# Performance work log

Hardware: AMD Instinct MI355X
Metric: run time of the kernel (lower is better)

The kernel has to match this reference:

```python
import jax, jax.numpy as jnp
import numpy as np


def setup_inputs() -> dict:
    key = jax.random.key(0)
    k1, k2 = jax.random.split(key)
    B, N, C = 4, 4096, 128
    points = jax.random.normal(k1, (B, N, 3), dtype=jnp.float32)
    features = jax.random.normal(k2, (B, C, N), dtype=jnp.float32)
    return {"points": points, "features": features, "npoint": 1024}


def _square_dist(a, b):
    # a: [B, N, D], b: [B, M, D] -> [B, N, M], norm=False (no division by D)
    aa = jnp.sum(a * a, axis=-1)  # [B, N]
    bb = jnp.sum(b * b, axis=-1)  # [B, M]
    ab = jnp.einsum('bnd,bmd->bnm', a, b)  # [B, N, M]
    return aa[:, :, None] + bb[:, None, :] - 2.0 * ab


def _fps_with_dist(dist, npoint):
    # dist: [B, N, N] pairwise squared distances; sequential furthest-point selection
    B, N, _ = dist.shape

    def step(carry, _):
        mind, last = carry  # mind: [B, N] min dist to selected set; last: [B] last picked idx
        d = jnp.take_along_axis(dist, last[:, None, None], axis=1)[:, 0, :]  # [B, N]
        mind = jnp.minimum(mind, d)
        nxt = jnp.argmax(mind, axis=1).astype(jnp.int32)
        return (mind, nxt), last

    init = (jnp.full((B, N), 1e10, dtype=dist.dtype), jnp.zeros((B,), jnp.int32))
    _, idxs = jax.lax.scan(step, init, None, length=npoint)  # [npoint, B]
    return idxs.T  # [B, npoint]


def reference(points, features, npoint):
    # features_for_fps = cat([points, features^T], dim=2): [B, N, 3 + C]
    f = jnp.concatenate([points, jnp.swapaxes(features, 1, 2)], axis=2)
    dist = _square_dist(f, f)  # [B, N, N]
    return _fps_with_dist(dist, npoint)
```

## Files before the change

kernel.cpp:

```cpp
#include <hip/hip_runtime.h>

#define BB 4
#define NN 4096
#define CC 128
#define DD 131
#define NPOINT 1024

__device__ __forceinline__ float fmul_(float a, float b) { return __fmul_rn(a, b); }
__device__ __forceinline__ float fadd_(float a, float b) { return __fadd_rn(a, b); }

__device__ float aa_xla_vf8ic4(const float* __restrict__ row) {
    float p[4][8];
#pragma unroll
    for (int j = 0; j < 4; ++j)
#pragma unroll
        for (int l = 0; l < 8; ++l)
            p[j][l] = fmul_(row[8 * j + l], row[8 * j + l]);
#pragma unroll
    for (int it = 1; it < 4; ++it)
#pragma unroll
        for (int j = 0; j < 4; ++j)
#pragma unroll
            for (int l = 0; l < 8; ++l) {
                float x = row[32 * it + 8 * j + l];
                p[j][l] = fadd_(p[j][l], fmul_(x, x));
            }
    float v[8];
#pragma unroll
    for (int l = 0; l < 8; ++l)
        v[l] = fadd_(fadd_(fadd_(p[0][l], p[1][l]), p[2][l]), p[3][l]);
    float h4_0 = fadd_(v[0], v[4]), h4_1 = fadd_(v[1], v[5]);
    float h4_2 = fadd_(v[2], v[6]), h4_3 = fadd_(v[3], v[7]);
    float h2_0 = fadd_(h4_0, h4_2), h2_1 = fadd_(h4_1, h4_3);
    float h1 = fadd_(h2_0, h2_1);
    h1 = fadd_(h1, fmul_(row[128], row[128]));
    h1 = fadd_(h1, fmul_(row[129], row[129]));
    h1 = fadd_(h1, fmul_(row[130], row[130]));
    return h1;
}

__global__ __launch_bounds__(256) void dist_kernel(const float* __restrict__ points,
                                                   const float* __restrict__ features,
                                                   float* __restrict__ dist) {
    __shared__ float At[64][132];
    __shared__ float Bt[32][132];
    __shared__ float s_aai[64];
    __shared__ float s_aaj[32];

    const int b  = blockIdx.z;
    const int i0 = blockIdx.x * 64;
    const int j0 = blockIdx.y * 32;
    const int tid = threadIdx.x;

    {
        const int rA = tid & 63, gA = tid >> 6;
        for (int k = gA; k < DD; k += 4) {
            float v;
            if (k < 3) v = points[((size_t)b * NN + i0 + rA) * 3 + k];
            else       v = features[((size_t)b * CC + (k - 3)) * NN + i0 + rA];
            At[rA][k] = v;
        }
        const int rB = tid & 31, gB = tid >> 5;
        for (int k = gB; k < DD; k += 8) {
            float v;
            if (k < 3) v = points[((size_t)b * NN + j0 + rB) * 3 + k];
            else       v = features[((size_t)b * CC + (k - 3)) * NN + j0 + rB];
            Bt[rB][k] = v;
        }
    }
    __syncthreads();

    if (tid < 64)        s_aai[tid]      = aa_xla_vf8ic4(At[tid]);
    else if (tid < 96)   s_aaj[tid - 64] = aa_xla_vf8ic4(Bt[tid - 64]);
    __syncthreads();

    const int tx = tid & 15;
    const int ty = tid >> 4;

    float acc[4][2];
#pragma unroll
    for (int p = 0; p < 4; ++p) { acc[p][0] = 0.f; acc[p][1] = 0.f; }

    for (int kb = 0; kb < 128; kb += 4) {
        float4 a0 = *(const float4*)&At[4 * ty + 0][kb];
        float4 a1 = *(const float4*)&At[4 * ty + 1][kb];
        float4 a2 = *(const float4*)&At[4 * ty + 2][kb];
        float4 a3 = *(const float4*)&At[4 * ty + 3][kb];
        float4 b0 = *(const float4*)&Bt[2 * tx + 0][kb];
        float4 b1 = *(const float4*)&Bt[2 * tx + 1][kb];
        const float4 av[4] = {a0, a1, a2, a3};
        const float4 bv[2] = {b0, b1};
#pragma unroll
        for (int p = 0; p < 4; ++p)
#pragma unroll
            for (int q = 0; q < 2; ++q) {
                float s = acc[p][q];
                s = __builtin_fmaf(av[p].x, bv[q].x, s);
                s = __builtin_fmaf(av[p].y, bv[q].y, s);
                s = __builtin_fmaf(av[p].z, bv[q].z, s);
                s = __builtin_fmaf(av[p].w, bv[q].w, s);
                acc[p][q] = s;
            }
    }
#pragma unroll
    for (int p = 0; p < 4; ++p)
#pragma unroll
        for (int q = 0; q < 2; ++q) {
            float s = acc[p][q];
            s = __builtin_fmaf(At[4 * ty + p][128], Bt[2 * tx + q][128], s);
            s = __builtin_fmaf(At[4 * ty + p][129], Bt[2 * tx + q][129], s);
            s = __builtin_fmaf(At[4 * ty + p][130], Bt[2 * tx + q][130], s);
            acc[p][q] = s;
        }

#pragma unroll
    for (int p = 0; p < 4; ++p) {
        const int i = i0 + 4 * ty + p;
        float2 st;
        st.x = __builtin_fmaf(-2.0f, acc[p][0],
                              fadd_(s_aai[4 * ty + p], s_aaj[2 * tx + 0]));
        st.y = __builtin_fmaf(-2.0f, acc[p][1],
                              fadd_(s_aai[4 * ty + p], s_aaj[2 * tx + 1]));
        *(float2*)&dist[((size_t)b * NN + i) * NN + j0 + 2 * tx] = st;
    }
}

__global__ __launch_bounds__(256) void fps_kernel(const float* __restrict__ dist,
                                                  int* __restrict__ out) {
    const int b = blockIdx.x;
    const int tid = threadIdx.x;
    const int lane = tid & 63;
    const int wave = tid >> 6;
    const float* Dm = dist + (size_t)b * NN * NN;

    __shared__ float s_val[2][4];
    __shared__ int   s_idx[2][4];

    float4 mind[4];
#pragma unroll
    for (int c = 0; c < 4; ++c) mind[c] = make_float4(1e10f, 1e10f, 1e10f, 1e10f);
    int last = 0;

    for (int k = 0; k < NPOINT; ++k) {
        if (tid == 0) out[b * NPOINT + k] = last;

        const float* row = Dm + (size_t)last * NN;
        float4 d[4];
#pragma unroll
        for (int c = 0; c < 4; ++c)
            d[c] = *(const float4*)&row[c * 1024 + 4 * tid];

#pragma unroll
        for (int c = 0; c < 4; ++c) {
            mind[c].x = fminf(mind[c].x, d[c].x);
            mind[c].y = fminf(mind[c].y, d[c].y);
            mind[c].z = fminf(mind[c].z, d[c].z);
            mind[c].w = fminf(mind[c].w, d[c].w);
        }

        float bv = mind[0].x; int bi = 4 * tid;
#pragma unroll
        for (int c = 0; c < 4; ++c) {
            const int base = c * 1024 + 4 * tid;
            const float* m = &mind[c].x;
#pragma unroll
            for (int e = 0; e < 4; ++e) {
                if (c == 0 && e == 0) continue;
                if (m[e] > bv) { bv = m[e]; bi = base + e; }
            }
        }

#pragma unroll
        for (int m = 32; m >= 1; m >>= 1) {
            float ov = __shfl_xor(bv, m, 64);
            int   oi = __shfl_xor(bi, m, 64);
            if (ov > bv || (ov == bv && oi < bi)) { bv = ov; bi = oi; }
        }

        const int p = k & 1;
        if (lane == 0) { s_val[p][wave] = bv; s_idx[p][wave] = bi; }
        __syncthreads();

        float v = s_val[p][lane & 3];
        int  ii = s_idx[p][lane & 3];
#pragma unroll
        for (int m = 2; m >= 1; m >>= 1) {
            float ov = __shfl_xor(v, m, 64);
            int   oi = __shfl_xor(ii, m, 64);
            if (ov > v || (ov == v && oi < ii)) { v = ov; ii = oi; }
        }
        last = ii;
    }
}

extern "C" void kernel_launch(void* const* d_in, const int* in_sizes, int n_in,
                              void* d_out, int out_size, void* d_ws, size_t ws_size,
                              hipStream_t stream) {
    const float* points   = (const float*)d_in[0];
    const float* features = (const float*)d_in[1];
    int* out = (int*)d_out;

    float* dist = (float*)d_ws;

    dim3 g(NN / 64, NN / 32, BB);
    dist_kernel<<<g, 256, 0, stream>>>(points, features, dist);

    fps_kernel<<<BB, 256, 0, stream>>>(dist, out);
}
```

Measured before the change: 1.838 ms.

## Retile distance GEMM to 64x64 k-major tiles and single-wave FPS

The distance kernel now uses 64x64 output tiles held k-major in shared memory and splits the 131-wide reduction into two staged halves. Each thread computes a 4x4 block and writes float4 stores. The squared-norm sums are computed in the same order as before, so results should be bit-identical. The FPS kernel drops from four waves to one wave per batch, with each lane holding 64 min-distances; this removes the per-iteration __syncthreads and cross-wave reduction but serialises more load and compare work per lane.

Measured after the change: 2.303 ms. +25.3%, slower.

```diff
diff --git a/kernel.cpp b/kernel.cpp
--- a/kernel.cpp
+++ b/kernel.cpp
@@ -9,159 +9,174 @@
 __device__ __forceinline__ float fmul_(float a, float b) { return __fmul_rn(a, b); }
 __device__ __forceinline__ float fadd_(float a, float b) { return __fadd_rn(a, b); }
 
-__device__ float aa_xla_vf8ic4(const float* __restrict__ row) {
-    float p[4][8];
-#pragma unroll
-    for (int j = 0; j < 4; ++j)
-#pragma unroll
-        for (int l = 0; l < 8; ++l)
-            p[j][l] = fmul_(row[8 * j + l], row[8 * j + l]);
-#pragma unroll
-    for (int it = 1; it < 4; ++it)
-#pragma unroll
-        for (int j = 0; j < 4; ++j)
-#pragma unroll
-            for (int l = 0; l < 8; ++l) {
-                float x = row[32 * it + 8 * j + l];
-                p[j][l] = fadd_(p[j][l], fmul_(x, x));
-            }
-    float v[8];
-#pragma unroll
-    for (int l = 0; l < 8; ++l)
-        v[l] = fadd_(fadd_(fadd_(p[0][l], p[1][l]), p[2][l]), p[3][l]);
-    float h4_0 = fadd_(v[0], v[4]), h4_1 = fadd_(v[1], v[5]);
-    float h4_2 = fadd_(v[2], v[6]), h4_3 = fadd_(v[3], v[7]);
-    float h2_0 = fadd_(h4_0, h4_2), h2_1 = fadd_(h4_1, h4_3);
-    float h1 = fadd_(h2_0, h2_1);
-    h1 = fadd_(h1, fmul_(row[128], row[128]));
-    h1 = fadd_(h1, fmul_(row[129], row[129]));
-    h1 = fadd_(h1, fmul_(row[130], row[130]));
-    return h1;
-}
-
 __global__ __launch_bounds__(256) void dist_kernel(const float* __restrict__ points,
                                                    const float* __restrict__ features,
                                                    float* __restrict__ dist) {
-    __shared__ float At[64][132];
-    __shared__ float Bt[32][132];
+    __shared__ float As[67][64];
+    __shared__ float Bs[67][64];
     __shared__ float s_aai[64];
-    __shared__ float s_aaj[32];
+    __shared__ float s_aaj[64];
 
     const int b  = blockIdx.z;
     const int i0 = blockIdx.x * 64;
-    const int j0 = blockIdx.y * 32;
+    const int j0 = blockIdx.y * 64;
     const int tid = threadIdx.x;
-
-    {
-        const int rA = tid & 63, gA = tid >> 6;
-        for (int k = gA; k < DD; k += 4) {
-            float v;
-            if (k < 3) v = points[((size_t)b * NN + i0 + rA) * 3 + k];
-            else       v = features[((size_t)b * CC + (k - 3)) * NN + i0 + rA];
-            At[rA][k] = v;
-        }
-        const int rB = tid & 31, gB = tid >> 5;
-        for (int k = gB; k < DD; k += 8) {
-            float v;
-            if (k < 3) v = points[((size_t)b * NN + j0 + rB) * 3 + k];
-            else       v = features[((size_t)b * CC + (k - 3)) * NN + j0 + rB];
-            Bt[rB][k] = v;
-        }
-    }
-    __syncthreads();
-
-    if (tid < 64)        s_aai[tid]      = aa_xla_vf8ic4(At[tid]);
-    else if (tid < 96)   s_aaj[tid - 64] = aa_xla_vf8ic4(Bt[tid - 64]);
-    __syncthreads();
-
+    const int r = tid & 63, g = tid >> 6;
     const int tx = tid & 15;
     const int ty = tid >> 4;
 
-    float acc[4][2];
-#pragma unroll
-    for (int p = 0; p < 4; ++p) { acc[p][0] = 0.f; acc[p][1] = 0.f; }
-
-    for (int kb = 0; kb < 128; kb += 4) {
-        float4 a0 = *(const float4*)&At[4 * ty + 0][kb];
-        float4 a1 = *(const float4*)&At[4 * ty + 1][kb];
-        float4 a2 = *(const float4*)&At[4 * ty + 2][kb];
-        float4 a3 = *(const float4*)&At[4 * ty + 3][kb];
-        float4 b0 = *(const float4*)&Bt[2 * tx + 0][kb];
-        float4 b1 = *(const float4*)&Bt[2 * tx + 1][kb];
-        const float4 av[4] = {a0, a1, a2, a3};
-        const float4 bv[2] = {b0, b1};
+    for (int k = g; k < 64; k += 4) {
+        float av, bv;
+        if (k < 3) {
+            av = points[((size_t)b * NN + i0 + r) * 3 + k];
+            bv = points[((size_t)b * NN + j0 + r) * 3 + k];
+        } else {
+            const float* frow = features + ((size_t)b * CC + (k - 3)) * NN;
+            av = frow[i0 + r];
+            bv = frow[j0 + r];
+        }
+        As[k][r] = av;
+        Bs[k][r] = bv;
+    }
+    __syncthreads();
+
+    float ph[4][8];
+    if (tid < 128) {
+        const int rr = tid & 63;
+        const float (*S)[64] = (tid < 64) ? As : Bs;
+#pragma unroll
+        for (int j = 0; j < 4; ++j)
+#pragma unroll
+            for (int l = 0; l < 8; ++l) {
+                float x = S[8 * j + l][rr];
+                ph[j][l] = fmul_(x, x);
+            }
+#pragma unroll
+        for (int j = 0; j < 4; ++j)
+#pragma unroll
+            for (int l = 0; l < 8; ++l) {
+                float x = S[32 + 8 * j + l][rr];
+                ph[j][l] = fadd_(ph[j][l], fmul_(x, x));
+            }
+    }
+
+    float acc[4][4];
+#pragma unroll
+    for (int p = 0; p < 4; ++p)
+#pragma unroll
+        for (int q = 0; q < 4; ++q) acc[p][q] = 0.f;
+
+#pragma unroll 4
+    for (int kk = 0; kk < 64; ++kk) {
+        float4 a4 = *(const float4*)&As[kk][4 * ty];
+        float4 b4 = *(const float4*)&Bs[kk][4 * tx];
+        const float a[4] = {a4.x, a4.y, a4.z, a4.w};
+        const float c[4] = {b4.x, b4.y, b4.z, b4.w};
 #pragma unroll
         for (int p = 0; p < 4; ++p)
 #pragma unroll
-            for (int q = 0; q < 2; ++q) {
-                float s = acc[p][q];
-                s = __builtin_fmaf(av[p].x, bv[q].x, s);
-                s = __builtin_fmaf(av[p].y, bv[q].y, s);
-                s = __builtin_fmaf(av[p].z, bv[q].z, s);
-                s = __builtin_fmaf(av[p].w, bv[q].w, s);
-                acc[p][q] = s;
-            }
-    }
-#pragma unroll
-    for (int p = 0; p < 4; ++p)
-#pragma unroll
-        for (int q = 0; q < 2; ++q) {
-            float s = acc[p][q];
-            s = __builtin_fmaf(At[4 * ty + p][128], Bt[2 * tx + q][128], s);
-            s = __builtin_fmaf(At[4 * ty + p][129], Bt[2 * tx + q][129], s);
-            s = __builtin_fmaf(At[4 * ty + p][130], Bt[2 * tx + q][130], s);
-            acc[p][q] = s;
-        }
+            for (int q = 0; q < 4; ++q)
+                acc[p][q] = __builtin_fmaf(a[p], c[q], acc[p][q]);
+    }
+    __syncthreads();
+
+    for (int k = g; k < 67; k += 4) {
+        const float* frow = features + ((size_t)b * CC + (64 + k - 3)) * NN;
+        As[k][r] = frow[i0 + r];
+        Bs[k][r] = frow[j0 + r];
+    }
+    __syncthreads();
+
+    if (tid < 128) {
+        const int rr = tid & 63;
+        const float (*S)[64] = (tid < 64) ? As : Bs;
+#pragma unroll
+        for (int j = 0; j < 4; ++j)
+#pragma unroll
+            for (int l = 0; l < 8; ++l) {
+                float x = S[8 * j + l][rr];
+                ph[j][l] = fadd_(ph[j][l], fmul_(x, x));
+            }
+#pragma unroll
+        for (int j = 0; j < 4; ++j)
+#pragma unroll
+            for (int l = 0; l < 8; ++l) {
+                float x = S[32 + 8 * j + l][rr];
+                ph[j][l] = fadd_(ph[j][l], fmul_(x, x));
+            }
+        float v[8];
+#pragma unroll
+        for (int l = 0; l < 8; ++l)
+            v[l] = fadd_(fadd_(fadd_(ph[0][l], ph[1][l]), ph[2][l]), ph[3][l]);
+        float h4_0 = fadd_(v[0], v[4]), h4_1 = fadd_(v[1], v[5]);
+        float h4_2 = fadd_(v[2], v[6]), h4_3 = fadd_(v[3], v[7]);
+        float h1 = fadd_(fadd_(h4_0, h4_2), fadd_(h4_1, h4_3));
+        float t0 = S[64][rr], t1 = S[65][rr], t2 = S[66][rr];
+        h1 = fadd_(h1, fmul_(t0, t0));
+        h1 = fadd_(h1, fmul_(t1, t1));
+        h1 = fadd_(h1, fmul_(t2, t2));
+        if (tid < 64) s_aai[rr] = h1; else s_aaj[rr] = h1;
+    }
+
+#pragma unroll 4
+    for (int kk = 0; kk < 67; ++kk) {
+        float4 a4 = *(const float4*)&As[kk][4 * ty];
+        float4 b4 = *(const float4*)&Bs[kk][4 * tx];
+        const float a[4] = {a4.x, a4.y, a4.z, a4.w};
+        const float c[4] = {b4.x, b4.y, b4.z, b4.w};
+#pragma unroll
+        for (int p = 0; p < 4; ++p)
+#pragma unroll
+            for (int q = 0; q < 4; ++q)
+                acc[p][q] = __builtin_fmaf(a[p], c[q], acc[p][q]);
+    }
+    __syncthreads();
 
 #pragma unroll
     for (int p = 0; p < 4; ++p) {
         const int i = i0 + 4 * ty + p;
-        float2 st;
-        st.x = __builtin_fmaf(-2.0f, acc[p][0],
-                              fadd_(s_aai[4 * ty + p], s_aaj[2 * tx + 0]));
-        st.y = __builtin_fmaf(-2.0f, acc[p][1],
-                              fadd_(s_aai[4 * ty + p], s_aaj[2 * tx + 1]));
-        *(float2*)&dist[((size_t)b * NN + i) * NN + j0 + 2 * tx] = st;
+        const float aai = s_aai[4 * ty + p];
+        float4 o;
+        o.x = __builtin_fmaf(-2.0f, acc[p][0], fadd_(aai, s_aaj[4 * tx + 0]));
+        o.y = __builtin_fmaf(-2.0f, acc[p][1], fadd_(aai, s_aaj[4 * tx + 1]));
+        o.z = __builtin_fmaf(-2.0f, acc[p][2], fadd_(aai, s_aaj[4 * tx + 2]));
+        o.w = __builtin_fmaf(-2.0f, acc[p][3], fadd_(aai, s_aaj[4 * tx + 3]));
+        *(float4*)&dist[((size_t)b * NN + i) * NN + j0 + 4 * tx] = o;
     }
 }
 
-__global__ __launch_bounds__(256) void fps_kernel(const float* __restrict__ dist,
-                                                  int* __restrict__ out) {
+__global__ __launch_bounds__(64, 1) void fps_kernel(const float* __restrict__ dist,
+                                                    int* __restrict__ out) {
     const int b = blockIdx.x;
-    const int tid = threadIdx.x;
-    const int lane = tid & 63;
-    const int wave = tid >> 6;
+    const int lane = threadIdx.x;
     const float* Dm = dist + (size_t)b * NN * NN;
 
-    __shared__ float s_val[2][4];
-    __shared__ int   s_idx[2][4];
-
-    float4 mind[4];
-#pragma unroll
-    for (int c = 0; c < 4; ++c) mind[c] = make_float4(1e10f, 1e10f, 1e10f, 1e10f);
+    float4 mind[16];
+#pragma unroll
+    for (int c = 0; c < 16; ++c) mind[c] = make_float4(1e10f, 1e10f, 1e10f, 1e10f);
     int last = 0;
 
     for (int k = 0; k < NPOINT; ++k) {
-        if (tid == 0) out[b * NPOINT + k] = last;
+        if (lane == 0) out[b * NPOINT + k] = last;
 
         const float* row = Dm + (size_t)last * NN;
-        float4 d[4];
-#pragma unroll
-        for (int c = 0; c < 4; ++c)
-            d[c] = *(const float4*)&row[c * 1024 + 4 * tid];
-
-#pragma unroll
-        for (int c = 0; c < 4; ++c) {
+        float4 d[16];
+#pragma unroll
+        for (int c = 0; c < 16; ++c)
+            d[c] = *(const float4*)&row[256 * c + 4 * lane];
+
+#pragma unroll
+        for (int c = 0; c < 16; ++c) {
             mind[c].x = fminf(mind[c].x, d[c].x);
             mind[c].y = fminf(mind[c].y, d[c].y);
             mind[c].z = fminf(mind[c].z, d[c].z);
             mind[c].w = fminf(mind[c].w, d[c].w);
         }
 
-        float bv = mind[0].x; int bi = 4 * tid;
-#pragma unroll
-        for (int c = 0; c < 4; ++c) {
-            const int base = c * 1024 + 4 * tid;
+        float bv = mind[0].x; int bi = 4 * lane;
+#pragma unroll
+        for (int c = 0; c < 16; ++c) {
+            const int base = 256 * c + 4 * lane;
             const float* m = &mind[c].x;
 #pragma unroll
             for (int e = 0; e < 4; ++e) {
@@ -176,20 +191,7 @@
             int   oi = __shfl_xor(bi, m, 64);
             if (ov > bv || (ov == bv && oi < bi)) { bv = ov; bi = oi; }
         }
-
-        const int p = k & 1;
-        if (lane == 0) { s_val[p][wave] = bv; s_idx[p][wave] = bi; }
-        __syncthreads();
-
-        float v = s_val[p][lane & 3];
-        int  ii = s_idx[p][lane & 3];
-#pragma unroll
-        for (int m = 2; m >= 1; m >>= 1) {
-            float ov = __shfl_xor(v, m, 64);
-            int   oi = __shfl_xor(ii, m, 64);
-            if (ov > v || (ov == v && oi < ii)) { v = ov; ii = oi; }
-        }
-        last = ii;
+        last = bi;
     }
 }
 
@@ -202,8 +204,8 @@
 
     float* dist = (float*)d_ws;
 
-    dim3 g(NN / 64, NN / 32, BB);
+    dim3 g(NN / 64, NN / 64, BB);
     dist_kernel<<<g, 256, 0, stream>>>(points, features, dist);
 
-    fps_kernel<<<BB, 256, 0, stream>>>(dist, out);
+    fps_kernel<<<BB, 64, 0, stream>>>(dist, out);
 }
```
